# Kernel optimization log

Measured on AMD Instinct MI355X. Metric: run time of the kernel, lower is better.

## Reference

```python
import jax, jax.numpy as jnp
import numpy as np

B, C, S = 16, 8, 128
DT, DX, DY = 0.001, 1.0, 1.0
NUM_STEPS = 10
EPS = 1e-6


def _thomas(a, b, c, d):
    """Batched Thomas tridiagonal solve. a,b,c,d: [M,N] rows; solve along N."""
    aT, bT, cT, dT = a.T, b.T, c.T, d.T  # [N, M]
    zero = jnp.zeros_like(dT[0])

    def fwd(carry, inp):
        cs_p, ds_p = carry
        ai, bi, ci, di = inp
        denom = bi - ai * cs_p + EPS  # i=0: cs_p=0 -> denom = b0 + eps (matches torch)
        cs = ci / denom
        ds = (di - ai * ds_p) / denom
        return (cs, ds), (cs, ds)

    _, (c_star, d_star) = jax.lax.scan(fwd, (zero, zero), (aT, bT, cT, dT))

    def bwd(x_next, inp):
        ci, di = inp
        x = di - ci * x_next
        return x, x

    _, xs = jax.lax.scan(bwd, d_star[-1], (c_star[:-1], d_star[:-1]), reverse=True)
    x = jnp.concatenate([xs, d_star[-1:]], axis=0)  # [N, M]
    return x.T


def _diffuse_rows(u2d, coeff):
    """Implicit 1D diffusion along last axis. u2d, coeff: [M,N]."""
    a = -coeff
    c = -coeff
    b = 1.0 + 2.0 * coeff
    b = b.at[:, 0].set(1.0 + coeff[:, 0])
    b = b.at[:, -1].set(1.0 + coeff[:, -1])
    return _thomas(a, b, c, u2d)


def _forward(u, alpha_base, beta_base, alpha_time_coeff, beta_time_coeff, channel_mixing):
    Bb, Cc, H, W = u.shape
    half = DT / 2.0
    t = 0.0
    for _ in range(NUM_STEPS):
        # x half-step (coefficient alpha at time t)
        alpha = jnp.clip(alpha_base + alpha_time_coeff * t, EPS, 10.0)
        u = jnp.einsum('dc,bchw->bdhw', channel_mixing, u)
        uf = u.reshape(Bb * Cc, H, W)
        af = jnp.broadcast_to(alpha[None], (Bb, Cc, H, W)).reshape(Bb * Cc, H, W)
        uf = _diffuse_rows(uf.reshape(-1, W), af.reshape(-1, W) * half / DX**2).reshape(Bb * Cc, H, W)
        t += half
        # y full step (coefficient beta at time t+dt/2)
        beta = jnp.clip(beta_base + beta_time_coeff * t, EPS, 10.0)
        bf = jnp.broadcast_to(beta[None], (Bb, Cc, H, W)).reshape(Bb * Cc, H, W)
        ut = uf.transpose(0, 2, 1).reshape(-1, H)
        bt = bf.transpose(0, 2, 1).reshape(-1, H)
        ut = _diffuse_rows(ut, bt * DT / DY**2)
        uf = ut.reshape(Bb * Cc, W, H).transpose(0, 2, 1)
        t += half
        # x half-step (coefficient alpha at time t+dt)
        alpha = jnp.clip(alpha_base + alpha_time_coeff * t, EPS, 10.0)
        af = jnp.broadcast_to(alpha[None], (Bb, Cc, H, W)).reshape(Bb * Cc, H, W)
        uf = _diffuse_rows(uf.reshape(-1, W), af.reshape(-1, W) * half / DX**2).reshape(Bb * Cc, H, W)
        u = uf.reshape(Bb, Cc, H, W)
    return u


def setup_inputs() -> dict:
    key = jax.random.key(0)
    k_u, k_cm, k_atc, k_btc = jax.random.split(key, 4)
    u = jax.random.normal(k_u, (B, C, S, S), dtype=jnp.float32)
    alpha_base = jnp.ones((C, S, S), dtype=jnp.float32)
    beta_base = jnp.ones((C, S, S), dtype=jnp.float32)
    alpha_time_coeff = jax.random.normal(k_atc, (C, S, S), dtype=jnp.float32) * 0.01
    beta_time_coeff = jax.random.normal(k_btc, (C, S, S), dtype=jnp.float32) * 0.01
    channel_mixing = jnp.eye(C, dtype=jnp.float32) + jax.random.normal(k_cm, (C, C), dtype=jnp.float32) * 0.01
    return {
        'u': u,
        'alpha_base': alpha_base,
        'beta_base': beta_base,
        'alpha_time_coeff': alpha_time_coeff,
        'beta_time_coeff': beta_time_coeff,
        'channel_mixing': channel_mixing,
    }


def reference(u, alpha_base, beta_base, alpha_time_coeff, beta_time_coeff, channel_mixing):
    return _forward(u, alpha_base, beta_base, alpha_time_coeff, beta_time_coeff, channel_mixing)
```

## Files before the change

kernel.cpp:

```cpp
#include <hip/hip_runtime.h>
#include <hip/hip_fp16.h>


constexpr int S_  = 128;
constexpr float EPSF = 1e-6f;
constexpr int CSS = 8 * 128 * 128;

constexpr int SA = 0;
constexpr int SB = 64 * 128;
constexpr int SC = 128 * 128;
constexpr int SPOOL = 192 * 128;
constexpr int HA  = 0;
constexpr int HST = 96 * 128;
constexpr int HB  = 96 * 128;
constexpr int HC  = 192 * 128;
constexpr int HPOOL = 256 * 128;

__device__ __forceinline__ int swad4(int r, int b4) {
    return r * 128 + (((b4) ^ (r & 31)) << 2);
}
__device__ __forceinline__ int swadw(int r, int w) {
    return r * 128 + ((((w) >> 2) ^ (r & 31)) << 2) + ((w) & 3);
}

template <int N>
__device__ __forceinline__ void jrunN(const float (&e)[N], const float (&g)[N],
                                      float (&o)[N - 4]) {
    float x1[N];
    #pragma unroll
    for (int i = 1; i <= N - 2; ++i) x1[i] = fmaf(g[i], e[i - 1] + e[i + 1], e[i]);
    #pragma unroll
    for (int i = 2; i <= N - 3; ++i) o[i - 2] = fmaf(g[i], x1[i - 1] + x1[i + 1], e[i]);
}

#define TAPS2(RA, RC, f, gt)                                                   \
    {                                                                          \
        _Pragma("unroll")                                                      \
        for (int i_ = 0; i_ < 4; ++i_) {                                       \
            const int bb_ = 2 * wr - 1 + i_;                                   \
            if (bb_ >= 0 && bb_ < 32) {                                        \
                const float4 va_ = *(const float4*)&sP[(RA) + swad4(r, bb_)];  \
                const float4 vc_ = *(const float4*)&sP[(RC) + swad4(r, bb_)];  \
                f[4*i_+0]=va_.x; f[4*i_+1]=va_.y; f[4*i_+2]=va_.z; f[4*i_+3]=va_.w; \
                gt[4*i_+0]=vc_.x; gt[4*i_+1]=vc_.y; gt[4*i_+2]=vc_.z; gt[4*i_+3]=vc_.w; \
            } else {                                                           \
                f[4*i_+0]=f[4*i_+1]=f[4*i_+2]=f[4*i_+3]=0.f;                   \
                gt[4*i_+0]=gt[4*i_+1]=gt[4*i_+2]=gt[4*i_+3]=0.f;               \
            }                                                                  \
        }                                                                      \
    }

__global__ __launch_bounds__(256) void coef_kernel(
    const float* __restrict__ ab, const float* __restrict__ atc,
    const float* __restrict__ bb, const float* __restrict__ btc,
    __half* __restrict__ cg)
{
    for (int gc = blockIdx.x * 256 + threadIdx.x; gc < CSS; gc += gridDim.x * 256) {
        const int w = gc & 127, h = (gc >> 7) & 127;
        const float abv = ab[gc], atv = atc[gc], bbv = bb[gc], btv = btc[gc];
        const float nbY = (h == 0 || h == S_ - 1) ? 1.f : 2.f;
        const float nbX = (w == 0 || w == S_ - 1) ? 1.f : 2.f;
        #pragma unroll
        for (int k = 0; k < 10; ++k) {
            float be = fminf(fmaxf(fmaf(btv, (2 * k + 1) * 0.0005f, bbv), EPSF), 10.f);
            float co = be * 0.001f;
            float rb = __builtin_amdgcn_rcpf(fmaf(nbY, co, 1.f) + EPSF);
            cg[k * CSS + gc] = __float2half(rb * co);
            float al = fminf(fmaxf(fmaf(atv, (2 * k + 2) * 0.0005f, abv), EPSF), 10.f);
            co = al * 0.0005f;
            rb = __builtin_amdgcn_rcpf(fmaf(nbX, co, 1.f) + EPSF);
            cg[(10 + k) * CSS + gc] = __float2half(rb * co);
        }
    }
}

__global__ __launch_bounds__(512) void head_kernel(
    const float* __restrict__ u0, __half* __restrict__ ud,
    const float* __restrict__ ab, const __half* __restrict__ cgy,
    const __half* __restrict__ cgx, const float* __restrict__ cm)
{
    __shared__ __align__(16) float sP[HPOOL];
    const int tid = threadIdx.x;
    const int b   = blockIdx.x >> 4;
    const int h0  = (blockIdx.x & 15) << 3;

    #pragma unroll
    for (int m = 0; m < 6; ++m) {
        const int task = tid + 512 * m;
        const int r = task >> 5, b4 = task & 31;
        const int c = r / 12, hh = r - c * 12;
        const int gh = h0 - 2 + hh;
        float4 v = make_float4(0.f, 0.f, 0.f, 0.f);
        if (gh >= 0 && gh < S_) v = *(const float4*)&u0[((b * 8 + c) * S_ + gh) * S_ + 4 * b4];
        *(float4*)&sP[HST + swad4(r, b4)] = v;
    }
    __syncthreads();
    {
        float M[64];
        #pragma unroll
        for (int i = 0; i < 64; ++i) M[i] = cm[i];
        #pragma unroll
        for (int m = 0; m < 3; ++m) {
            const int p = tid + 512 * m;
            const int hh = p >> 7, w = p & 127;
            float v[8], o[8];
            #pragma unroll
            for (int c = 0; c < 8; ++c) v[c] = sP[HST + swadw(c * 12 + hh, w)];
            #pragma unroll
            for (int dd = 0; dd < 8; ++dd) {
                float a = 0.f;
                #pragma unroll
                for (int c = 0; c < 8; ++c) a = fmaf(M[dd * 8 + c], v[c], a);
                o[dd] = a;
            }
            #pragma unroll
            for (int c = 0; c < 8; ++c) sP[HST + swadw(c * 12 + hh, w)] = o[c];
        }
    }
    __syncthreads();
    {
        float xh[3][8];
        #pragma unroll
        for (int m = 0; m < 3; ++m) {
            const int r  = (tid & 31) + 32 * m;
            const int wr = tid >> 5;
            const int w0 = wr * 8;
            const int c = r / 12, hh = r - c * 12;
            const int gh = h0 - 2 + hh;
            const bool rowin = (gh >= 0 && gh < S_);
            float f[16];
            #pragma unroll
            for (int i = 0; i < 4; ++i) {
                const int bb4 = 2 * wr - 1 + i;
                if (bb4 >= 0 && bb4 < 32) {
                    const float4 va = *(const float4*)&sP[HST + swad4(r, bb4)];
                    f[4*i+0]=va.x; f[4*i+1]=va.y; f[4*i+2]=va.z; f[4*i+3]=va.w;
                } else {
                    f[4*i+0]=f[4*i+1]=f[4*i+2]=f[4*i+3]=0.f;
                }
            }
            float e[12], g[12];
            #pragma unroll
            for (int j = 0; j < 12; ++j) {
                const int wj = w0 - 2 + j;
                const bool win = (wj >= 0 && wj < S_);
                float co = 0.f;
                if (rowin && win) {
                    float al = ab[(c * S_ + gh) * S_ + wj];
                    co = fminf(fmaxf(al, EPSF), 10.f) * 0.0005f;
                }
                const float nb = (wj == 0 || wj == S_ - 1) ? 1.f : 2.f;
                const float rb = __builtin_amdgcn_rcpf(fmaf(nb, co, 1.f) + EPSF);
                e[j] = rb * f[j + 2]; g[j] = rb * co;
            }
            jrunN<12>(e, g, xh[m]);
        }
        __syncthreads();
        #pragma unroll
        for (int m = 0; m < 3; ++m) {
            const int r  = (tid & 31) + 32 * m;
            const int wr = tid >> 5;
            *(float4*)&sP[HST + swad4(r, 2 * wr)]     = make_float4(xh[m][0], xh[m][1], xh[m][2], xh[m][3]);
            *(float4*)&sP[HST + swad4(r, 2 * wr + 1)] = make_float4(xh[m][4], xh[m][5], xh[m][6], xh[m][7]);
        }
    }
    __syncthreads();
    {
        const int c = tid >> 6, wp = tid & 63, wb = 2 * wp;
        float2 dp[12]; uint dg[12];
        #pragma unroll
        for (int hh = 0; hh < 12; ++hh) {
            const int gh = h0 - 2 + hh;
            const bool inr = (gh >= 0 && gh < S_);
            const int ghc = inr ? gh : 0;
            const int r = c * 12 + hh;
            dp[hh] = *(const float2*)&sP[HST + r * 128 +
                                         (((wp >> 1) ^ (r & 31)) << 2) + 2 * (wp & 1)];
            dg[hh] = *(const uint*)&cgy[(c * S_ + ghc) * S_ + wb];
        }
        float o2[2][8];
        #pragma unroll
        for (int s = 0; s < 2; ++s) {
            float e[12], g[12];
            #pragma unroll
            for (int hh = 0; hh < 12; ++hh) {
                const int gh = h0 - 2 + hh;
                const bool inr = (gh >= 0 && gh < S_);
                uint gb = dg[hh];
                __half2 hg = *reinterpret_cast<__half2*>(&gb);
                float gv = s ? __high2float(hg) : __low2float(hg);
                gv = inr ? gv : 0.f;
                const float nb = (gh == 0 || gh == S_ - 1) ? 1.f : 2.f;
                const float rb = fmaf(-nb, gv, 1.f);
                e[hh] = rb * (s ? dp[hh].y : dp[hh].x);
                g[hh] = gv;
            }
            jrunN<12>(e, g, o2[s]);
        }
        #pragma unroll
        for (int i = 0; i < 8; ++i) {
            const int r = c * 8 + i;
            *(float2*)&sP[HA + r * 128 + (((wp >> 1) ^ (r & 31)) << 2) + 2 * (wp & 1)]
                = make_float2(o2[0][i], o2[1][i]);
        }
    }
    {
        const ushort* cx = (const ushort*)cgx;
        #pragma unroll
        for (int m = 0; m < 4; ++m) {
            const int task = tid + 512 * m;
            const int r = task >> 5, b4 = task & 31;
            const int c = r >> 3, ho = r & 7;
            const uint2 v = *(const uint2*)&cx[(c * S_ + h0 + ho) * S_ + b4 * 4];
            uint lo = v.x, hi = v.y;
            __half2 h0_ = *reinterpret_cast<__half2*>(&lo);
            __half2 h1_ = *reinterpret_cast<__half2*>(&hi);
            *(float4*)&sP[HC + swad4(r, b4)] = make_float4(
                __low2float(h0_), __high2float(h0_), __low2float(h1_), __high2float(h1_));
        }
    }
    __syncthreads();
    float rbk[2][12], gk[2][12], xo[2][8];
    #pragma unroll
    for (int m = 0; m < 2; ++m) {
        const int r  = tid & 63;
        const int wr = (tid >> 6) + 8 * m;
        const int w0 = wr * 8;
        float f[16], gt[16];
        TAPS2(HA, HC, f, gt)
        float e[12];
        #pragma unroll
        for (int j = 0; j < 12; ++j) {
            const int wj = w0 - 2 + j;
            const float nb = (wj == 0 || wj == S_ - 1) ? 1.f : 2.f;
            gk[m][j] = gt[j + 2];
            rbk[m][j] = fmaf(-nb, gt[j + 2], 1.f);
            e[j] = rbk[m][j] * f[j + 2];
        }
        jrunN<12>(e, gk[m], xo[m]);
    }
    #pragma unroll
    for (int m = 0; m < 2; ++m) {
        const int r  = tid & 63;
        const int wr = (tid >> 6) + 8 * m;
        *(float4*)&sP[HB + swad4(r, 2 * wr)]     = make_float4(xo[m][0], xo[m][1], xo[m][2], xo[m][3]);
        *(float4*)&sP[HB + swad4(r, 2 * wr + 1)] = make_float4(xo[m][4], xo[m][5], xo[m][6], xo[m][7]);
    }
    __syncthreads();
    {
        float M[64];
        #pragma unroll
        for (int i = 0; i < 64; ++i) M[i] = cm[i];
        #pragma unroll
        for (int m = 0; m < 2; ++m) {
            const int p = tid + 512 * m;
            const int ho = p >> 7, w = p & 127;
            float v[8], o[8];
            #pragma unroll
            for (int c = 0; c < 8; ++c) v[c] = sP[HB + swadw(c * 8 + ho, w)];
            #pragma unroll
            for (int dd = 0; dd < 8; ++dd) {
                float a = 0.f;
                #pragma unroll
                for (int c = 0; c < 8; ++c) a = fmaf(M[dd * 8 + c], v[c], a);
                o[dd] = a;
            }
            #pragma unroll
            for (int c = 0; c < 8; ++c) sP[HA + swadw(c * 8 + ho, w)] = o[c];
        }
    }
    __syncthreads();
    #pragma unroll
    for (int m = 0; m < 2; ++m) {
        const int r  = tid & 63;
        const int wr = (tid >> 6) + 8 * m;
        const int c = r >> 3, ho = r & 7;
        float f[16];
        #pragma unroll
        for (int i = 0; i < 4; ++i) {
            const int bb4 = 2 * wr - 1 + i;
            if (bb4 >= 0 && bb4 < 32) {
                const float4 va = *(const float4*)&sP[HA + swad4(r, bb4)];
                f[4*i+0]=va.x; f[4*i+1]=va.y; f[4*i+2]=va.z; f[4*i+3]=va.w;
            } else {
                f[4*i+0]=f[4*i+1]=f[4*i+2]=f[4*i+3]=0.f;
            }
        }
        float e[12];
        #pragma unroll
        for (int j = 0; j < 12; ++j) e[j] = rbk[m][j] * f[j + 2];
        float o[8]; jrunN<12>(e, gk[m], o);
        __half2 q0 = __floats2half2_rn(o[0], o[1]);
        __half2 q1 = __floats2half2_rn(o[2], o[3]);
        __half2 q2 = __floats2half2_rn(o[4], o[5]);
        __half2 q3 = __floats2half2_rn(o[6], o[7]);
        uint4 pk;
        pk.x = *reinterpret_cast<uint*>(&q0);
        pk.y = *reinterpret_cast<uint*>(&q1);
        pk.z = *reinterpret_cast<uint*>(&q2);
        pk.w = *reinterpret_cast<uint*>(&q3);
        *(uint4*)&ud[((b * 8 + c) * S_ + h0 + ho) * S_ + wr * 8] = pk;
    }
}

template <bool LASTK>
__global__ __launch_bounds__(512) void stepS_kernel(
    const __half* __restrict__ us, void* __restrict__ udst_,
    const __half* __restrict__ cgy, const __half* __restrict__ cgx,
    const float* __restrict__ cm)
{
    __shared__ __align__(16) float sP[SPOOL];
    const int tid = threadIdx.x;
    const int b   = blockIdx.x >> 4;
    const int h0  = (blockIdx.x & 15) << 3;

    {
        const int c = tid >> 6, wp = tid & 63, wb = 2 * wp;
        uint du[12], dg[12];
        #pragma unroll
        for (int hh = 0; hh < 12; ++hh) {
            const int gh = h0 - 2 + hh;
            const bool inr = (gh >= 0 && gh < S_);
            const int ghc = inr ? gh : 0;
            du[hh] = inr ? *(const uint*)&us[((b * 8 + c) * S_ + ghc) * S_ + wb] : 0u;
            dg[hh] = *(const uint*)&cgy[(c * S_ + ghc) * S_ + wb];
        }
        float o2[2][8];
        #pragma unroll
        for (int s = 0; s < 2; ++s) {
            float e[12], g[12];
            #pragma unroll
            for (int hh = 0; hh < 12; ++hh) {
                const int gh = h0 - 2 + hh;
                const bool inr = (gh >= 0 && gh < S_);
                uint ub = du[hh];
                __half2 hu = *reinterpret_cast<__half2*>(&ub);
                const float dv = s ? __high2float(hu) : __low2float(hu);
                uint gb = dg[hh];
                __half2 hg = *reinterpret_cast<__half2*>(&gb);
                float gv = s ? __high2float(hg) : __low2float(hg);
                gv = inr ? gv : 0.f;
                const float nb = (gh == 0 || gh == S_ - 1) ? 1.f : 2.f;
                const float rb = fmaf(-nb, gv, 1.f);
                e[hh] = rb * dv;
                g[hh] = gv;
            }
            jrunN<12>(e, g, o2[s]);
        }
        #pragma unroll
        for (int i = 0; i < 8; ++i) {
            const int r = c * 8 + i;
            *(float2*)&sP[SA + r * 128 + (((wp >> 1) ^ (r & 31)) << 2) + 2 * (wp & 1)]
                = make_float2(o2[0][i], o2[1][i]);
        }
    }
    {
        const ushort* cx = (const ushort*)cgx;
        #pragma unroll
        for (int m = 0; m < 4; ++m) {
            const int task = tid + 512 * m;
            const int r = task >> 5, b4 = task & 31;
            const int c = r >> 3, ho = r & 7;
            const uint2 v = *(const uint2*)&cx[(c * S_ + h0 + ho) * S_ + b4 * 4];
            uint lo = v.x, hi = v.y;
            __half2 h0_ = *reinterpret_cast<__half2*>(&lo);
            __half2 h1_ = *reinterpret_cast<__half2*>(&hi);
            *(float4*)&sP[SC + swad4(r, b4)] = make_float4(
                __low2float(h0_), __high2float(h0_), __low2float(h1_), __high2float(h1_));
        }
    }
    __syncthreads();

    float rbk[2][12], gk[2][12], xo[2][8];
    #pragma unroll
    for (int m = 0; m < 2; ++m) {
        const int r  = tid & 63;
        const int wr = (tid >> 6) + 8 * m;
        const int w0 = wr * 8;
        float f[16], gt[16];
        TAPS2(SA, SC, f, gt)
        float e[12];
        #pragma unroll
        for (int j = 0; j < 12; ++j) {
            const int wj = w0 - 2 + j;
            const float nb = (wj == 0 || wj == S_ - 1) ? 1.f : 2.f;
            gk[m][j] = gt[j + 2];
            rbk[m][j] = fmaf(-nb, gt[j + 2], 1.f);
            e[j] = rbk[m][j] * f[j + 2];
        }
        jrunN<12>(e, gk[m], xo[m]);
    }

    if (LASTK) {
        float* ud = (float*)udst_;
        #pragma unroll
        for (int m = 0; m < 2; ++m) {
            const int r  = tid & 63;
            const int wr = (tid >> 6) + 8 * m;
            const int c = r >> 3, ho = r & 7;
            float4* dst4 = (float4*)&ud[((b * 8 + c) * S_ + h0 + ho) * S_ + wr * 8];
            dst4[0] = make_float4(xo[m][0], xo[m][1], xo[m][2], xo[m][3]);
            dst4[1] = make_float4(xo[m][4], xo[m][5], xo[m][6], xo[m][7]);
        }
    } else {
        #pragma unroll
        for (int m = 0; m < 2; ++m) {
            const int r  = tid & 63;
            const int wr = (tid >> 6) + 8 * m;
            *(float4*)&sP[SB + swad4(r, 2 * wr)]     = make_float4(xo[m][0], xo[m][1], xo[m][2], xo[m][3]);
            *(float4*)&sP[SB + swad4(r, 2 * wr + 1)] = make_float4(xo[m][4], xo[m][5], xo[m][6], xo[m][7]);
        }
        __syncthreads();
        {
            float M[64];
            #pragma unroll
            for (int i = 0; i < 64; ++i) M[i] = cm[i];
            #pragma unroll
            for (int m = 0; m < 2; ++m) {
                const int p = tid + 512 * m;
                const int ho = p >> 7, w = p & 127;
                float v[8], o[8];
                #pragma unroll
                for (int c = 0; c < 8; ++c) v[c] = sP[SB + swadw(c * 8 + ho, w)];
                #pragma unroll
                for (int dd = 0; dd < 8; ++dd) {
                    float a = 0.f;
                    #pragma unroll
                    for (int c = 0; c < 8; ++c) a = fmaf(M[dd * 8 + c], v[c], a);
                    o[dd] = a;
                }
                #pragma unroll
                for (int c = 0; c < 8; ++c) sP[SA + swadw(c * 8 + ho, w)] = o[c];
            }
        }
        __syncthreads();
        __half* ud = (__half*)udst_;
        #pragma unroll
        for (int m = 0; m < 2; ++m) {
            const int r  = tid & 63;
            const int wr = (tid >> 6) + 8 * m;
            const int c = r >> 3, ho = r & 7;
            float f[16];
            #pragma unroll
            for (int i = 0; i < 4; ++i) {
                const int bb4 = 2 * wr - 1 + i;
                if (bb4 >= 0 && bb4 < 32) {
                    const float4 va = *(const float4*)&sP[SA + swad4(r, bb4)];
                    f[4*i+0]=va.x; f[4*i+1]=va.y; f[4*i+2]=va.z; f[4*i+3]=va.w;
                } else {
                    f[4*i+0]=f[4*i+1]=f[4*i+2]=f[4*i+3]=0.f;
                }
            }
            float e[12];
            #pragma unroll
            for (int j = 0; j < 12; ++j) e[j] = rbk[m][j] * f[j + 2];
            float o[8]; jrunN<12>(e, gk[m], o);
            __half2 q0 = __floats2half2_rn(o[0], o[1]);
            __half2 q1 = __floats2half2_rn(o[2], o[3]);
            __half2 q2 = __floats2half2_rn(o[4], o[5]);
            __half2 q3 = __floats2half2_rn(o[6], o[7]);
            uint4 pk;
            pk.x = *reinterpret_cast<uint*>(&q0);
            pk.y = *reinterpret_cast<uint*>(&q1);
            pk.z = *reinterpret_cast<uint*>(&q2);
            pk.w = *reinterpret_cast<uint*>(&q3);
            *(uint4*)&ud[((b * 8 + c) * S_ + h0 + ho) * S_ + wr * 8] = pk;
        }
    }
}

extern "C" void kernel_launch(void* const* d_in, const int* in_sizes, int n_in,
                              void* d_out, int out_size, void* d_ws, size_t ws_size,
                              hipStream_t stream) {
    const float* u_in = (const float*)d_in[0];
    const float* ab   = (const float*)d_in[1];
    const float* bbta = (const float*)d_in[2];
    const float* atc  = (const float*)d_in[3];
    const float* btc  = (const float*)d_in[4];
    const float* cm   = (const float*)d_in[5];
    float* uo = (float*)d_out;
    __half* h1 = (__half*)d_ws;
    __half* h2 = (__half*)((char*)d_ws + (8u << 20));
    __half* cg = (__half*)((char*)d_ws + (16u << 20));

    coef_kernel<<<dim3(512), dim3(256), 0, stream>>>(ab, atc, bbta, btc, cg);

    const dim3 g(256), blk(512);
    head_kernel<<<g, blk, 0, stream>>>(u_in, h1, ab, cg + 0 * CSS,
                                       cg + 10 * CSS, cm);
    const __half* s = h1; __half* d = h2;
    for (int k = 1; k <= 8; ++k) {
        stepS_kernel<false><<<g, blk, 0, stream>>>(s, d, cg + k * CSS,
                                                   cg + (10 + k) * CSS, cm);
        const __half* ns = d;
        d = (d == h2) ? h1 : h2;
        s = ns;
    }
    stepS_kernel<true><<<g, blk, 0, stream>>>(s, uo, cg + 9 * CSS,
                                              cg + 19 * CSS, cm);
}
```

Measured before the change: 156.1 us.

## Fuse coefficient precompute into head kernel and store packed (g, rb-1) half2 pairs

Removes the separate coef_kernel launch. The head kernel now computes its own step-0 coefficients inline from the raw alpha/beta inputs, and at its tail writes coefficients for steps 1-9 as half2 pairs holding (rb*co, rb-1). Step kernels read these precomputed pairs instead of rebuilding rb from g and boundary flags. This saves one launch and some ALU work per step, but doubles the size of the coefficient stream read by each step kernel. Coefficient writes at the end of the head kernel may also lengthen its critical path.

```diff
diff --git a/kernel.cpp b/kernel.cpp
--- a/kernel.cpp
+++ b/kernel.cpp
@@ -33,7 +33,7 @@
     for (int i = 2; i <= N - 3; ++i) o[i - 2] = fmaf(g[i], x1[i - 1] + x1[i + 1], e[i]);
 }
 
-#define TAPS2(RA, RC, f, gt)                                                   \
+#define TAPS_GATHER(RA, RC, f, cb)                                             \
     {                                                                          \
         _Pragma("unroll")                                                      \
         for (int i_ = 0; i_ < 4; ++i_) {                                       \
@@ -42,47 +42,26 @@
                 const float4 va_ = *(const float4*)&sP[(RA) + swad4(r, bb_)];  \
                 const float4 vc_ = *(const float4*)&sP[(RC) + swad4(r, bb_)];  \
                 f[4*i_+0]=va_.x; f[4*i_+1]=va_.y; f[4*i_+2]=va_.z; f[4*i_+3]=va_.w; \
-                gt[4*i_+0]=vc_.x; gt[4*i_+1]=vc_.y; gt[4*i_+2]=vc_.z; gt[4*i_+3]=vc_.w; \
+                cb[4*i_+0]=__float_as_uint(vc_.x); cb[4*i_+1]=__float_as_uint(vc_.y); \
+                cb[4*i_+2]=__float_as_uint(vc_.z); cb[4*i_+3]=__float_as_uint(vc_.w); \
             } else {                                                           \
                 f[4*i_+0]=f[4*i_+1]=f[4*i_+2]=f[4*i_+3]=0.f;                   \
-                gt[4*i_+0]=gt[4*i_+1]=gt[4*i_+2]=gt[4*i_+3]=0.f;               \
+                cb[4*i_+0]=cb[4*i_+1]=cb[4*i_+2]=cb[4*i_+3]=0u;                \
             }                                                                  \
         }                                                                      \
     }
 
-__global__ __launch_bounds__(256) void coef_kernel(
+__global__ __launch_bounds__(512) void head_kernel(
+    const float* __restrict__ u0, __half* __restrict__ ud,
     const float* __restrict__ ab, const float* __restrict__ atc,
     const float* __restrict__ bb, const float* __restrict__ btc,
-    __half* __restrict__ cg)
-{
-    for (int gc = blockIdx.x * 256 + threadIdx.x; gc < CSS; gc += gridDim.x * 256) {
-        const int w = gc & 127, h = (gc >> 7) & 127;
-        const float abv = ab[gc], atv = atc[gc], bbv = bb[gc], btv = btc[gc];
-        const float nbY = (h == 0 || h == S_ - 1) ? 1.f : 2.f;
-        const float nbX = (w == 0 || w == S_ - 1) ? 1.f : 2.f;
-        #pragma unroll
-        for (int k = 0; k < 10; ++k) {
-            float be = fminf(fmaxf(fmaf(btv, (2 * k + 1) * 0.0005f, bbv), EPSF), 10.f);
-            float co = be * 0.001f;
-            float rb = __builtin_amdgcn_rcpf(fmaf(nbY, co, 1.f) + EPSF);
-            cg[k * CSS + gc] = __float2half(rb * co);
-            float al = fminf(fmaxf(fmaf(atv, (2 * k + 2) * 0.0005f, abv), EPSF), 10.f);
-            co = al * 0.0005f;
-            rb = __builtin_amdgcn_rcpf(fmaf(nbX, co, 1.f) + EPSF);
-            cg[(10 + k) * CSS + gc] = __float2half(rb * co);
-        }
-    }
-}
-
-__global__ __launch_bounds__(512) void head_kernel(
-    const float* __restrict__ u0, __half* __restrict__ ud,
-    const float* __restrict__ ab, const __half* __restrict__ cgy,
-    const __half* __restrict__ cgx, const float* __restrict__ cm)
+    const float* __restrict__ cm, __half2* __restrict__ cf)
 {
     __shared__ __align__(16) float sP[HPOOL];
     const int tid = threadIdx.x;
     const int b   = blockIdx.x >> 4;
     const int h0  = (blockIdx.x & 15) << 3;
+    const float dt2 = 0.0005f;
 
     #pragma unroll
     for (int m = 0; m < 6; ++m) {
@@ -167,7 +146,7 @@
     __syncthreads();
     {
         const int c = tid >> 6, wp = tid & 63, wb = 2 * wp;
-        float2 dp[12]; uint dg[12];
+        float2 dp[12], b2[12], t2[12];
         #pragma unroll
         for (int hh = 0; hh < 12; ++hh) {
             const int gh = h0 - 2 + hh;
@@ -176,7 +155,8 @@
             const int r = c * 12 + hh;
             dp[hh] = *(const float2*)&sP[HST + r * 128 +
                                          (((wp >> 1) ^ (r & 31)) << 2) + 2 * (wp & 1)];
-            dg[hh] = *(const uint*)&cgy[(c * S_ + ghc) * S_ + wb];
+            b2[hh] = *(const float2*)&bb[(c * S_ + ghc) * S_ + wb];
+            t2[hh] = *(const float2*)&btc[(c * S_ + ghc) * S_ + wb];
         }
         float o2[2][8];
         #pragma unroll
@@ -186,14 +166,13 @@
             for (int hh = 0; hh < 12; ++hh) {
                 const int gh = h0 - 2 + hh;
                 const bool inr = (gh >= 0 && gh < S_);
-                uint gb = dg[hh];
-                __half2 hg = *reinterpret_cast<__half2*>(&gb);
-                float gv = s ? __high2float(hg) : __low2float(hg);
-                gv = inr ? gv : 0.f;
+                float be = fmaf(s ? t2[hh].y : t2[hh].x, 1 * dt2, s ? b2[hh].y : b2[hh].x);
+                be = fminf(fmaxf(be, EPSF), 10.f);
+                const float co = inr ? be * 0.001f : 0.f;
                 const float nb = (gh == 0 || gh == S_ - 1) ? 1.f : 2.f;
-                const float rb = fmaf(-nb, gv, 1.f);
+                const float rb = __builtin_amdgcn_rcpf(fmaf(nb, co, 1.f) + EPSF);
                 e[hh] = rb * (s ? dp[hh].y : dp[hh].x);
-                g[hh] = gv;
+                g[hh] = rb * co;
             }
             jrunN<12>(e, g, o2[s]);
         }
@@ -204,20 +183,29 @@
                 = make_float2(o2[0][i], o2[1][i]);
         }
     }
-    {
-        const ushort* cx = (const ushort*)cgx;
-        #pragma unroll
-        for (int m = 0; m < 4; ++m) {
-            const int task = tid + 512 * m;
-            const int r = task >> 5, b4 = task & 31;
-            const int c = r >> 3, ho = r & 7;
-            const uint2 v = *(const uint2*)&cx[(c * S_ + h0 + ho) * S_ + b4 * 4];
-            uint lo = v.x, hi = v.y;
-            __half2 h0_ = *reinterpret_cast<__half2*>(&lo);
-            __half2 h1_ = *reinterpret_cast<__half2*>(&hi);
-            *(float4*)&sP[HC + swad4(r, b4)] = make_float4(
-                __low2float(h0_), __high2float(h0_), __low2float(h1_), __high2float(h1_));
-        }
+    #pragma unroll
+    for (int m = 0; m < 4; ++m) {
+        const int task = tid + 512 * m;
+        const int r = task >> 5, b4 = task & 31;
+        const int c = r >> 3, ho = r & 7;
+        const float4 a4 = *(const float4*)&ab[(c * S_ + h0 + ho) * S_ + 4 * b4];
+        const float4 t4 = *(const float4*)&atc[(c * S_ + h0 + ho) * S_ + 4 * b4];
+        uint pk[4];
+        #pragma unroll
+        for (int l = 0; l < 4; ++l) {
+            const int w = 4 * b4 + l;
+            const float av = l == 0 ? a4.x : (l == 1 ? a4.y : (l == 2 ? a4.z : a4.w));
+            const float tv = l == 0 ? t4.x : (l == 1 ? t4.y : (l == 2 ? t4.z : t4.w));
+            float al = fminf(fmaxf(fmaf(tv, 2 * dt2, av), EPSF), 10.f);
+            const float co = al * 0.0005f;
+            const float nb = (w == 0 || w == S_ - 1) ? 1.f : 2.f;
+            const float rb = __builtin_amdgcn_rcpf(fmaf(nb, co, 1.f) + EPSF);
+            __half2 hp = __floats2half2_rn(rb * co, rb - 1.f);
+            pk[l] = *reinterpret_cast<uint*>(&hp);
+        }
+        *(float4*)&sP[HC + swad4(r, b4)] = make_float4(
+            __uint_as_float(pk[0]), __uint_as_float(pk[1]),
+            __uint_as_float(pk[2]), __uint_as_float(pk[3]));
     }
     __syncthreads();
     float rbk[2][12], gk[2][12], xo[2][8];
@@ -225,16 +213,14 @@
     for (int m = 0; m < 2; ++m) {
         const int r  = tid & 63;
         const int wr = (tid >> 6) + 8 * m;
-        const int w0 = wr * 8;
-        float f[16], gt[16];
-        TAPS2(HA, HC, f, gt)
+        float f[16]; uint cb[16];
+        TAPS_GATHER(HA, HC, f, cb)
         float e[12];
         #pragma unroll
         for (int j = 0; j < 12; ++j) {
-            const int wj = w0 - 2 + j;
-            const float nb = (wj == 0 || wj == S_ - 1) ? 1.f : 2.f;
-            gk[m][j] = gt[j + 2];
-            rbk[m][j] = fmaf(-nb, gt[j + 2], 1.f);
+            uint c_ = cb[j + 2];
+            const float2 fc = __half22float2(*reinterpret_cast<__half2*>(&c_));
+            rbk[m][j] = 1.f + fc.y; gk[m][j] = fc.x;
             e[j] = rbk[m][j] * f[j + 2];
         }
         jrunN<12>(e, gk[m], xo[m]);
@@ -301,12 +287,31 @@
         pk.w = *reinterpret_cast<uint*>(&q3);
         *(uint4*)&ud[((b * 8 + c) * S_ + h0 + ho) * S_ + wr * 8] = pk;
     }
+
+    {
+        const int idx = blockIdx.x * 512 + tid;
+        const float abv = ab[idx], atv = atc[idx], bbv = bb[idx], btv = btc[idx];
+        const int w = idx & 127, h = (idx >> 7) & 127;
+        const float nbY = (h == 0 || h == S_ - 1) ? 1.f : 2.f;
+        const float nbX = (w == 0 || w == S_ - 1) ? 1.f : 2.f;
+        #pragma unroll
+        for (int k = 1; k < 10; ++k) {
+            float be = fminf(fmaxf(fmaf(btv, (2 * k + 1) * dt2, bbv), EPSF), 10.f);
+            float co = be * 0.001f;
+            float rb = __builtin_amdgcn_rcpf(fmaf(nbY, co, 1.f) + EPSF);
+            cf[k * CSS + idx] = __floats2half2_rn(rb * co, rb - 1.f);
+            float al = fminf(fmaxf(fmaf(atv, (2 * k + 2) * dt2, abv), EPSF), 10.f);
+            co = al * 0.0005f;
+            rb = __builtin_amdgcn_rcpf(fmaf(nbX, co, 1.f) + EPSF);
+            cf[(10 + k) * CSS + idx] = __floats2half2_rn(rb * co, rb - 1.f);
+        }
+    }
 }
 
 template <bool LASTK>
 __global__ __launch_bounds__(512) void stepS_kernel(
     const __half* __restrict__ us, void* __restrict__ udst_,
-    const __half* __restrict__ cgy, const __half* __restrict__ cgx,
+    const __half2* __restrict__ cfy, const __half2* __restrict__ cfx,
     const float* __restrict__ cm)
 {
     __shared__ __align__(16) float sP[SPOOL];
@@ -315,15 +320,17 @@
     const int h0  = (blockIdx.x & 15) << 3;
 
     {
-        const int c = tid >> 6, wp = tid & 63, wb = 2 * wp;
-        uint du[12], dg[12];
+        const int c  = tid >> 6;
+        const int wp = tid & 63;
+        const int wbase = 2 * wp;
+        uint du[12]; uint2 dc[12];
         #pragma unroll
         for (int hh = 0; hh < 12; ++hh) {
             const int gh = h0 - 2 + hh;
             const bool inr = (gh >= 0 && gh < S_);
             const int ghc = inr ? gh : 0;
-            du[hh] = inr ? *(const uint*)&us[((b * 8 + c) * S_ + ghc) * S_ + wb] : 0u;
-            dg[hh] = *(const uint*)&cgy[(c * S_ + ghc) * S_ + wb];
+            du[hh] = inr ? *(const uint*)&us[((b * 8 + c) * S_ + ghc) * S_ + wbase] : 0u;
+            dc[hh] = *(const uint2*)&cfy[(c * S_ + ghc) * S_ + wbase];
         }
         float o2[2][8];
         #pragma unroll
@@ -336,14 +343,10 @@
                 uint ub = du[hh];
                 __half2 hu = *reinterpret_cast<__half2*>(&ub);
                 const float dv = s ? __high2float(hu) : __low2float(hu);
-                uint gb = dg[hh];
-                __half2 hg = *reinterpret_cast<__half2*>(&gb);
-                float gv = s ? __high2float(hg) : __low2float(hg);
-                gv = inr ? gv : 0.f;
-                const float nb = (gh == 0 || gh == S_ - 1) ? 1.f : 2.f;
-                const float rb = fmaf(-nb, gv, 1.f);
-                e[hh] = rb * dv;
-                g[hh] = gv;
+                uint cb = s ? dc[hh].y : dc[hh].x;
+                const float2 f = __half22float2(*reinterpret_cast<__half2*>(&cb));
+                e[hh] = (1.f + f.y) * dv;
+                g[hh] = inr ? f.x : 0.f;
             }
             jrunN<12>(e, g, o2[s]);
         }
@@ -355,18 +358,16 @@
         }
     }
     {
-        const ushort* cx = (const ushort*)cgx;
+        const uint* cfxu = (const uint*)cfx;
         #pragma unroll
         for (int m = 0; m < 4; ++m) {
             const int task = tid + 512 * m;
-            const int r = task >> 5, b4 = task & 31;
+            const int r = task >> 5, col4 = task & 31;
             const int c = r >> 3, ho = r & 7;
-            const uint2 v = *(const uint2*)&cx[(c * S_ + h0 + ho) * S_ + b4 * 4];
-            uint lo = v.x, hi = v.y;
-            __half2 h0_ = *reinterpret_cast<__half2*>(&lo);
-            __half2 h1_ = *reinterpret_cast<__half2*>(&hi);
-            *(float4*)&sP[SC + swad4(r, b4)] = make_float4(
-                __low2float(h0_), __high2float(h0_), __low2float(h1_), __high2float(h1_));
+            const uint4 v = *(const uint4*)&cfxu[(c * S_ + h0 + ho) * S_ + col4 * 4];
+            *(float4*)&sP[SC + swad4(r, col4)] =
+                make_float4(__uint_as_float(v.x), __uint_as_float(v.y),
+                            __uint_as_float(v.z), __uint_as_float(v.w));
         }
     }
     __syncthreads();
@@ -376,16 +377,14 @@
     for (int m = 0; m < 2; ++m) {
         const int r  = tid & 63;
         const int wr = (tid >> 6) + 8 * m;
-        const int w0 = wr * 8;
-        float f[16], gt[16];
-        TAPS2(SA, SC, f, gt)
+        float f[16]; uint cb[16];
+        TAPS_GATHER(SA, SC, f, cb)
         float e[12];
         #pragma unroll
         for (int j = 0; j < 12; ++j) {
-            const int wj = w0 - 2 + j;
-            const float nb = (wj == 0 || wj == S_ - 1) ? 1.f : 2.f;
-            gk[m][j] = gt[j + 2];
-            rbk[m][j] = fmaf(-nb, gt[j + 2], 1.f);
+            uint c_ = cb[j + 2];
+            const float2 fc = __half22float2(*reinterpret_cast<__half2*>(&c_));
+            rbk[m][j] = 1.f + fc.y; gk[m][j] = fc.x;
             e[j] = rbk[m][j] * f[j + 2];
         }
         jrunN<12>(e, gk[m], xo[m]);
@@ -407,8 +406,10 @@
         for (int m = 0; m < 2; ++m) {
             const int r  = tid & 63;
             const int wr = (tid >> 6) + 8 * m;
-            *(float4*)&sP[SB + swad4(r, 2 * wr)]     = make_float4(xo[m][0], xo[m][1], xo[m][2], xo[m][3]);
-            *(float4*)&sP[SB + swad4(r, 2 * wr + 1)] = make_float4(xo[m][4], xo[m][5], xo[m][6], xo[m][7]);
+            *(float4*)&sP[SB + swad4(r, 2 * wr)] =
+                make_float4(xo[m][0], xo[m][1], xo[m][2], xo[m][3]);
+            *(float4*)&sP[SB + swad4(r, 2 * wr + 1)] =
+                make_float4(xo[m][4], xo[m][5], xo[m][6], xo[m][7]);
         }
         __syncthreads();
         {
@@ -421,7 +422,10 @@
                 const int ho = p >> 7, w = p & 127;
                 float v[8], o[8];
                 #pragma unroll
-                for (int c = 0; c < 8; ++c) v[c] = sP[SB + swadw(c * 8 + ho, w)];
+                for (int c = 0; c < 8; ++c) {
+                    const int r = c * 8 + ho;
+                    v[c] = sP[SB + r * 128 + (((w >> 2) ^ (r & 31)) << 2) + (w & 3)];
+                }
                 #pragma unroll
                 for (int dd = 0; dd < 8; ++dd) {
                     float a = 0.f;
@@ -430,7 +434,10 @@
                     o[dd] = a;
                 }
                 #pragma unroll
-                for (int c = 0; c < 8; ++c) sP[SA + swadw(c * 8 + ho, w)] = o[c];
+                for (int c = 0; c < 8; ++c) {
+                    const int r = c * 8 + ho;
+                    sP[SA + r * 128 + (((w >> 2) ^ (r & 31)) << 2) + (w & 3)] = o[c];
+                }
             }
         }
         __syncthreads();
@@ -443,12 +450,13 @@
             float f[16];
             #pragma unroll
             for (int i = 0; i < 4; ++i) {
-                const int bb4 = 2 * wr - 1 + i;
-                if (bb4 >= 0 && bb4 < 32) {
-                    const float4 va = *(const float4*)&sP[SA + swad4(r, bb4)];
-                    f[4*i+0]=va.x; f[4*i+1]=va.y; f[4*i+2]=va.z; f[4*i+3]=va.w;
+                const int bb = 2 * wr - 1 + i;
+                if (bb >= 0 && bb < 32) {
+                    const float4 va = *(const float4*)&sP[SA + swad4(r, bb)];
+                    f[4 * i + 0] = va.x; f[4 * i + 1] = va.y;
+                    f[4 * i + 2] = va.z; f[4 * i + 3] = va.w;
                 } else {
-                    f[4*i+0]=f[4*i+1]=f[4*i+2]=f[4*i+3]=0.f;
+                    f[4 * i + 0] = f[4 * i + 1] = f[4 * i + 2] = f[4 * i + 3] = 0.f;
                 }
             }
             float e[12];
@@ -479,23 +487,20 @@
     const float* btc  = (const float*)d_in[4];
     const float* cm   = (const float*)d_in[5];
     float* uo = (float*)d_out;
-    __half* h1 = (__half*)d_ws;
-    __half* h2 = (__half*)((char*)d_ws + (8u << 20));
-    __half* cg = (__half*)((char*)d_ws + (16u << 20));
-
-    coef_kernel<<<dim3(512), dim3(256), 0, stream>>>(ab, atc, bbta, btc, cg);
+    __half*  h1 = (__half*)d_ws;
+    __half*  h2 = (__half*)((char*)d_ws + (8u << 20));
+    __half2* cf = (__half2*)((char*)d_ws + (16u << 20));
 
     const dim3 g(256), blk(512);
-    head_kernel<<<g, blk, 0, stream>>>(u_in, h1, ab, cg + 0 * CSS,
-                                       cg + 10 * CSS, cm);
+    head_kernel<<<g, blk, 0, stream>>>(u_in, h1, ab, atc, bbta, btc, cm, cf);
     const __half* s = h1; __half* d = h2;
     for (int k = 1; k <= 8; ++k) {
-        stepS_kernel<false><<<g, blk, 0, stream>>>(s, d, cg + k * CSS,
-                                                   cg + (10 + k) * CSS, cm);
+        stepS_kernel<false><<<g, blk, 0, stream>>>(s, d, cf + k * CSS,
+                                                   cf + (10 + k) * CSS, cm);
         const __half* ns = d;
         d = (d == h2) ? h1 : h2;
         s = ns;
     }
-    stepS_kernel<true><<<g, blk, 0, stream>>>(s, uo, cg + 9 * CSS,
-                                              cg + 19 * CSS, cm);
+    stepS_kernel<true><<<g, blk, 0, stream>>>(s, uo, cf + 9 * CSS,
+                                              cf + 19 * CSS, cm);
 }
```

Measured after the change: 156.7 us. About the same (+0.4%).
